# Optimization experiments

Hardware: AMD Instinct MI355X
Metric: run time of the kernel (lower is better)

## Reference

```python
import jax, jax.numpy as jnp
import numpy as np

N_LEVELS = 16
LOG2_T = 19
TABLE_SIZE = 1 << LOG2_T
F_PER_LEVEL = 2
BASE_RES = 16
MAX_RES = 4096
HASH_INIT_SCALE = 0.001
B = 524288

_GROWTH = np.exp((np.log(MAX_RES) - np.log(BASE_RES)) / (N_LEVELS - 1))
SCALINGS = jnp.asarray(np.floor(BASE_RES * _GROWTH ** np.arange(N_LEVELS)), dtype=jnp.float32)  # [L]
HASH_OFFSET = jnp.arange(N_LEVELS, dtype=jnp.int32) * TABLE_SIZE  # [L]
# Instant-NGP spatial hash primes; stored as uint32 so multiplication wraps mod 2^32
# (low 19 bits after xor are identical to torch's int64 computation followed by % 2^19).
PRIMES = jnp.array([1, 2654435761, 805459861], dtype=jnp.uint32)


def _hash_fn(coords_u32):
    # coords_u32: [..., L, 3] uint32 -> [..., L] int32 indices into flat table
    h = coords_u32 * PRIMES
    h = h[..., 0] ^ h[..., 1] ^ h[..., 2]
    h = (h & jnp.uint32(TABLE_SIZE - 1)).astype(jnp.int32)
    return h + HASH_OFFSET


def setup_inputs() -> dict:
    key = jax.random.key(0)
    k1, k2 = jax.random.split(key)
    in_tensor = jax.random.uniform(k1, (B, 3), dtype=jnp.float32)
    hash_table = (jax.random.uniform(k2, (TABLE_SIZE * N_LEVELS, F_PER_LEVEL),
                                     dtype=jnp.float32) * 2.0 - 1.0) * HASH_INIT_SCALE
    return {"in_tensor": in_tensor, "hash_table": hash_table}


def _hashgrid_forward(in_tensor, hash_table):
    # in_tensor: [B, 3] in [0,1]; hash_table: [L*T, F]
    scaled = in_tensor[:, None, :] * SCALINGS[None, :, None]  # [B, L, 3]
    c = jnp.ceil(scaled).astype(jnp.int32)   # ceil corners
    f = jnp.floor(scaled).astype(jnp.int32)  # floor corners
    offset = scaled - f.astype(scaled.dtype)  # [B, L, 3]

    cu = c.astype(jnp.uint32)
    fu = f.astype(jnp.uint32)

    def corner(x, y, z):
        idx = _hash_fn(jnp.stack([x, y, z], axis=-1))  # [B, L]
        return hash_table[idx]  # [B, L, F]

    # Corner ordering exactly as in the torch implementation
    f_0 = corner(cu[..., 0], cu[..., 1], cu[..., 2])
    f_1 = corner(cu[..., 0], fu[..., 1], cu[..., 2])
    f_2 = corner(fu[..., 0], fu[..., 1], cu[..., 2])
    f_3 = corner(fu[..., 0], cu[..., 1], cu[..., 2])
    f_4 = corner(cu[..., 0], cu[..., 1], fu[..., 2])
    f_5 = corner(cu[..., 0], fu[..., 1], fu[..., 2])
    f_6 = corner(fu[..., 0], fu[..., 1], fu[..., 2])
    f_7 = corner(fu[..., 0], cu[..., 1], fu[..., 2])

    ox = offset[..., 0:1]
    oy = offset[..., 1:2]
    oz = offset[..., 2:3]

    f_03 = f_0 * ox + f_3 * (1 - ox)
    f_12 = f_1 * ox + f_2 * (1 - ox)
    f_56 = f_5 * ox + f_6 * (1 - ox)
    f_47 = f_4 * ox + f_7 * (1 - ox)
    f0312 = f_03 * oy + f_12 * (1 - oy)
    f4756 = f_47 * oy + f_56 * (1 - oy)
    enc = f0312 * oz + f4756 * (1 - oz)  # [B, L, F]
    return enc.reshape(enc.shape[0], N_LEVELS * F_PER_LEVEL)  # [B, L*F]


def reference(in_tensor, hash_table):
    # c2f is None -> scale_grad_by_freq is the identity in forward
    return _hashgrid_forward(in_tensor, hash_table)
```

## Files before the change

kernel.cpp:

```cpp
#include <hip/hip_runtime.h>


typedef float f2 __attribute__((ext_vector_type(2)));
typedef float f4 __attribute__((ext_vector_type(4)));

#define TSZ_MASK  ((1u << 19) - 1u)
#define LOG2_B    19

static __constant__ float C_SCALE[16] = {
    16.f,  23.f,  33.f,   48.f,   70.f,   101.f,  147.f,  212.f,
    307.f, 445.f, 645.f,  933.f,  1351.f, 1955.f, 2830.f, 4095.f
};

__global__ __launch_bounds__(256) void hashgrid_gather(
    const float* __restrict__ in,
    const f2*    __restrict__ tab,
    f2*          __restrict__ scratch,
    int lvl0)
{
    const unsigned gid = blockIdx.x * 256 + threadIdx.x;
    const int lvl = lvl0 + (int)(gid >> LOG2_B);
    const unsigned p = gid & TSZ_MASK;

    const float x = __builtin_nontemporal_load(&in[p * 3 + 0]);
    const float y = __builtin_nontemporal_load(&in[p * 3 + 1]);
    const float z = __builtin_nontemporal_load(&in[p * 3 + 2]);
    const float s = C_SCALE[lvl];

    const float sx = x * s, sy = y * s, sz = z * s;
    const float fxf = floorf(sx), fyf = floorf(sy), fzf = floorf(sz);
    const float ox = sx - fxf, oy = sy - fyf, oz = sz - fzf;

    const unsigned fx = (unsigned)(int)fxf;
    const unsigned fy = (unsigned)(int)fyf;
    const unsigned fz = (unsigned)(int)fzf;
    const unsigned cx = (unsigned)(int)ceilf(sx);
    const unsigned cy = (unsigned)(int)ceilf(sy);
    const unsigned cz = (unsigned)(int)ceilf(sz);

    const unsigned hyc = cy * 2654435761u;
    const unsigned hyf = fy * 2654435761u;
    const unsigned hzc = cz * 805459861u;
    const unsigned hzf = fz * 805459861u;

    const f2* __restrict__ tl = tab + ((size_t)lvl << LOG2_B);

    const unsigned i0 = (cx ^ hyc ^ hzc) & TSZ_MASK;
    const unsigned i1 = (cx ^ hyf ^ hzc) & TSZ_MASK;
    const unsigned i2 = (fx ^ hyf ^ hzc) & TSZ_MASK;
    const unsigned i3 = (fx ^ hyc ^ hzc) & TSZ_MASK;
    const unsigned i4 = (cx ^ hyc ^ hzf) & TSZ_MASK;
    const unsigned i5 = (cx ^ hyf ^ hzf) & TSZ_MASK;
    const unsigned i6 = (fx ^ hyf ^ hzf) & TSZ_MASK;
    const unsigned i7 = (fx ^ hyc ^ hzf) & TSZ_MASK;

    const f2 f0 = tl[i0];
    const f2 f1 = tl[i1];
    const f2 f2_ = tl[i2];
    const f2 f3 = tl[i3];
    const f2 f4_ = tl[i4];
    const f2 f5 = tl[i5];
    const f2 f6 = tl[i6];
    const f2 f7 = tl[i7];

    const float rx = 1.f - ox, ry = 1.f - oy, rz = 1.f - oz;
    f2 e = ((f0 * ox + f3 * rx) * oy + (f1 * ox + f2_ * rx) * ry) * oz
         + ((f4_ * ox + f7 * rx) * oy + (f5 * ox + f6 * rx) * ry) * rz;

    __builtin_nontemporal_store(e, &scratch[((size_t)lvl << LOG2_B) + p]);
}

__global__ __launch_bounds__(256) void hashgrid_transpose(
    const f2* __restrict__ scratch,
    f4*       __restrict__ out)
{
    __shared__ f2 tile[64][17];
    const int t = threadIdx.x;
    const int lane = t & 63, w = t >> 6;
    const unsigned pbase = blockIdx.x * 64;

#pragma unroll
    for (int i = 0; i < 4; ++i) {
        const int lvl = w * 4 + i;
        tile[lane][lvl] = __builtin_nontemporal_load(
            &scratch[((size_t)lvl << LOG2_B) + pbase + lane]);
    }
    __syncthreads();

    const unsigned obase = blockIdx.x * 512;
#pragma unroll
    for (int rep = 0; rep < 2; ++rep) {
        const int j = t + rep * 256;
        const int pt = j >> 3, k = j & 7;
        const f2 a = tile[pt][2 * k];
        const f2 b = tile[pt][2 * k + 1];
        f4 v = {a.x, a.y, b.x, b.y};
        __builtin_nontemporal_store(v, &out[obase + j]);
    }
}

__global__ __launch_bounds__(256) void hashgrid_mono(
    const float* __restrict__ in, const f2* __restrict__ tab,
    f2* __restrict__ out, int nthreads)
{
    const int gid = blockIdx.x * 256 + threadIdx.x;
    if (gid >= nthreads) return;
    const int p = gid >> 4;
    const int lvl = gid & 15;

    const float x = in[p * 3 + 0];
    const float y = in[p * 3 + 1];
    const float z = in[p * 3 + 2];
    const float s = C_SCALE[lvl];

    const float sx = x * s, sy = y * s, sz = z * s;
    const float fxf = floorf(sx), fyf = floorf(sy), fzf = floorf(sz);
    const float ox = sx - fxf, oy = sy - fyf, oz = sz - fzf;

    const unsigned fx = (unsigned)(int)fxf, fy = (unsigned)(int)fyf,
                   fz = (unsigned)(int)fzf;
    const unsigned cx = (unsigned)(int)ceilf(sx), cy = (unsigned)(int)ceilf(sy),
                   cz = (unsigned)(int)ceilf(sz);

    const unsigned hyc = cy * 2654435761u, hyf = fy * 2654435761u;
    const unsigned hzc = cz * 805459861u,  hzf = fz * 805459861u;
    const unsigned base = (unsigned)lvl << 19;

    const unsigned i0 = ((cx ^ hyc ^ hzc) & TSZ_MASK) + base;
    const unsigned i1 = ((cx ^ hyf ^ hzc) & TSZ_MASK) + base;
    const unsigned i2 = ((fx ^ hyf ^ hzc) & TSZ_MASK) + base;
    const unsigned i3 = ((fx ^ hyc ^ hzc) & TSZ_MASK) + base;
    const unsigned i4 = ((cx ^ hyc ^ hzf) & TSZ_MASK) + base;
    const unsigned i5 = ((cx ^ hyf ^ hzf) & TSZ_MASK) + base;
    const unsigned i6 = ((fx ^ hyf ^ hzf) & TSZ_MASK) + base;
    const unsigned i7 = ((fx ^ hyc ^ hzf) & TSZ_MASK) + base;

    const f2 f0 = tab[i0], f1 = tab[i1], f2_ = tab[i2], f3 = tab[i3];
    const f2 f4_ = tab[i4], f5 = tab[i5], f6 = tab[i6], f7 = tab[i7];

    const float rx = 1.f - ox, ry = 1.f - oy, rz = 1.f - oz;
    f2 e = ((f0 * ox + f3 * rx) * oy + (f1 * ox + f2_ * rx) * ry) * oz
         + ((f4_ * ox + f7 * rx) * oy + (f5 * ox + f6 * rx) * ry) * rz;

    out[(p << 4) + lvl] = e;
}

extern "C" void kernel_launch(void* const* d_in, const int* in_sizes, int n_in,
                              void* d_out, int out_size, void* d_ws, size_t ws_size,
                              hipStream_t stream)
{
    const float* in  = (const float*)d_in[0];
    const f2*    tab = (const f2*)d_in[1];

    const int n_points = in_sizes[0] / 3;
    const size_t scratch_bytes = (size_t)16 * (1u << LOG2_B) * sizeof(f2);

    if (n_points == (1 << LOG2_B) && ws_size >= scratch_bytes) {
        f2* scratch = (f2*)d_ws;
        hipLaunchKernelGGL(hashgrid_gather, dim3((5u << LOG2_B) / 256), dim3(256),
                           0, stream, in, tab, scratch, 0);
        for (int l = 5; l < 16; ++l) {
            hipLaunchKernelGGL(hashgrid_gather, dim3((1u << LOG2_B) / 256), dim3(256),
                               0, stream, in, tab, scratch, l);
        }
        hipLaunchKernelGGL(hashgrid_transpose, dim3((1u << LOG2_B) / 64), dim3(256),
                           0, stream, scratch, (f4*)d_out);
    } else {
        const int nthreads = n_points * 16;
        hipLaunchKernelGGL(hashgrid_mono, dim3((nthreads + 255) / 256), dim3(256),
                           0, stream, in, tab, (f2*)d_out, nthreads);
    }
}
```

Measured before the change: 298.2 us.

## Merge per-level gather launches into one grid with two points per thread

Replaces the twelve gather launches (levels 0-4 together, then one per level) with a single launch of 16K blocks ordered level-major, where each thread handles two points of the same level. The two corner-index computations run before both trilinear gathers, so sixteen independent table loads are in flight per thread. This removes launch gaps between levels and raises memory-level parallelism. The risk is that all levels now run concurrently, so the L2 working set may grow, and register pressure rises. Corner hashing and interpolation are also factored into shared helpers that the fallback kernel reuses.

```diff
diff --git a/kernel.cpp b/kernel.cpp
--- a/kernel.cpp
+++ b/kernel.cpp
@@ -12,24 +12,20 @@
     307.f, 445.f, 645.f,  933.f,  1351.f, 1955.f, 2830.f, 4095.f
 };
 
-__global__ __launch_bounds__(256) void hashgrid_gather(
-    const float* __restrict__ in,
-    const f2*    __restrict__ tab,
-    f2*          __restrict__ scratch,
-    int lvl0)
+struct Corner8 { unsigned i[8]; float ox, oy, oz; };
+
+__device__ __forceinline__ Corner8 corner_idx(const float* __restrict__ in,
+                                              unsigned p, float s)
 {
-    const unsigned gid = blockIdx.x * 256 + threadIdx.x;
-    const int lvl = lvl0 + (int)(gid >> LOG2_B);
-    const unsigned p = gid & TSZ_MASK;
-
     const float x = __builtin_nontemporal_load(&in[p * 3 + 0]);
     const float y = __builtin_nontemporal_load(&in[p * 3 + 1]);
     const float z = __builtin_nontemporal_load(&in[p * 3 + 2]);
-    const float s = C_SCALE[lvl];
 
     const float sx = x * s, sy = y * s, sz = z * s;
     const float fxf = floorf(sx), fyf = floorf(sy), fzf = floorf(sz);
-    const float ox = sx - fxf, oy = sy - fyf, oz = sz - fzf;
+
+    Corner8 r;
+    r.ox = sx - fxf; r.oy = sy - fyf; r.oz = sz - fzf;
 
     const unsigned fx = (unsigned)(int)fxf;
     const unsigned fy = (unsigned)(int)fyf;
@@ -43,31 +39,46 @@
     const unsigned hzc = cz * 805459861u;
     const unsigned hzf = fz * 805459861u;
 
+    r.i[0] = (cx ^ hyc ^ hzc) & TSZ_MASK;
+    r.i[1] = (cx ^ hyf ^ hzc) & TSZ_MASK;
+    r.i[2] = (fx ^ hyf ^ hzc) & TSZ_MASK;
+    r.i[3] = (fx ^ hyc ^ hzc) & TSZ_MASK;
+    r.i[4] = (cx ^ hyc ^ hzf) & TSZ_MASK;
+    r.i[5] = (cx ^ hyf ^ hzf) & TSZ_MASK;
+    r.i[6] = (fx ^ hyf ^ hzf) & TSZ_MASK;
+    r.i[7] = (fx ^ hyc ^ hzf) & TSZ_MASK;
+    return r;
+}
+
+__device__ __forceinline__ f2 trilerp(const f2* __restrict__ tl, const Corner8& c)
+{
+    const f2 f0 = tl[c.i[0]], f1 = tl[c.i[1]], f2_ = tl[c.i[2]], f3 = tl[c.i[3]];
+    const f2 f4_ = tl[c.i[4]], f5 = tl[c.i[5]], f6 = tl[c.i[6]], f7 = tl[c.i[7]];
+    const float rx = 1.f - c.ox, ry = 1.f - c.oy, rz = 1.f - c.oz;
+    return ((f0 * c.ox + f3 * rx) * c.oy + (f1 * c.ox + f2_ * rx) * ry) * c.oz
+         + ((f4_ * c.ox + f7 * rx) * c.oy + (f5 * c.ox + f6 * rx) * ry) * rz;
+}
+
+__global__ __launch_bounds__(256) void hashgrid_gather(
+    const float* __restrict__ in,
+    const f2*    __restrict__ tab,
+    f2*          __restrict__ scratch)
+{
+    const unsigned b = blockIdx.x;
+    const int lvl = (int)(b >> 10);
+    const unsigned p0 = (b & 1023u) * 512u + threadIdx.x;
+    const unsigned p1 = p0 + 256u;
+    const float s = C_SCALE[lvl];
     const f2* __restrict__ tl = tab + ((size_t)lvl << LOG2_B);
 
-    const unsigned i0 = (cx ^ hyc ^ hzc) & TSZ_MASK;
-    const unsigned i1 = (cx ^ hyf ^ hzc) & TSZ_MASK;
-    const unsigned i2 = (fx ^ hyf ^ hzc) & TSZ_MASK;
-    const unsigned i3 = (fx ^ hyc ^ hzc) & TSZ_MASK;
-    const unsigned i4 = (cx ^ hyc ^ hzf) & TSZ_MASK;
-    const unsigned i5 = (cx ^ hyf ^ hzf) & TSZ_MASK;
-    const unsigned i6 = (fx ^ hyf ^ hzf) & TSZ_MASK;
-    const unsigned i7 = (fx ^ hyc ^ hzf) & TSZ_MASK;
+    const Corner8 ca = corner_idx(in, p0, s);
+    const Corner8 cb = corner_idx(in, p1, s);
+    const f2 ea = trilerp(tl, ca);
+    const f2 eb = trilerp(tl, cb);
 
-    const f2 f0 = tl[i0];
-    const f2 f1 = tl[i1];
-    const f2 f2_ = tl[i2];
-    const f2 f3 = tl[i3];
-    const f2 f4_ = tl[i4];
-    const f2 f5 = tl[i5];
-    const f2 f6 = tl[i6];
-    const f2 f7 = tl[i7];
-
-    const float rx = 1.f - ox, ry = 1.f - oy, rz = 1.f - oz;
-    f2 e = ((f0 * ox + f3 * rx) * oy + (f1 * ox + f2_ * rx) * ry) * oz
-         + ((f4_ * ox + f7 * rx) * oy + (f5 * ox + f6 * rx) * ry) * rz;
-
-    __builtin_nontemporal_store(e, &scratch[((size_t)lvl << LOG2_B) + p]);
+    f2* __restrict__ sl = scratch + ((size_t)lvl << LOG2_B);
+    __builtin_nontemporal_store(ea, &sl[p0]);
+    __builtin_nontemporal_store(eb, &sl[p1]);
 }
 
 __global__ __launch_bounds__(256) void hashgrid_transpose(
@@ -107,42 +118,10 @@
     if (gid >= nthreads) return;
     const int p = gid >> 4;
     const int lvl = gid & 15;
-
-    const float x = in[p * 3 + 0];
-    const float y = in[p * 3 + 1];
-    const float z = in[p * 3 + 2];
     const float s = C_SCALE[lvl];
-
-    const float sx = x * s, sy = y * s, sz = z * s;
-    const float fxf = floorf(sx), fyf = floorf(sy), fzf = floorf(sz);
-    const float ox = sx - fxf, oy = sy - fyf, oz = sz - fzf;
-
-    const unsigned fx = (unsigned)(int)fxf, fy = (unsigned)(int)fyf,
-                   fz = (unsigned)(int)fzf;
-    const unsigned cx = (unsigned)(int)ceilf(sx), cy = (unsigned)(int)ceilf(sy),
-                   cz = (unsigned)(int)ceilf(sz);
-
-    const unsigned hyc = cy * 2654435761u, hyf = fy * 2654435761u;
-    const unsigned hzc = cz * 805459861u,  hzf = fz * 805459861u;
-    const unsigned base = (unsigned)lvl << 19;
-
-    const unsigned i0 = ((cx ^ hyc ^ hzc) & TSZ_MASK) + base;
-    const unsigned i1 = ((cx ^ hyf ^ hzc) & TSZ_MASK) + base;
-    const unsigned i2 = ((fx ^ hyf ^ hzc) & TSZ_MASK) + base;
-    const unsigned i3 = ((fx ^ hyc ^ hzc) & TSZ_MASK) + base;
-    const unsigned i4 = ((cx ^ hyc ^ hzf) & TSZ_MASK) + base;
-    const unsigned i5 = ((cx ^ hyf ^ hzf) & TSZ_MASK) + base;
-    const unsigned i6 = ((fx ^ hyf ^ hzf) & TSZ_MASK) + base;
-    const unsigned i7 = ((fx ^ hyc ^ hzf) & TSZ_MASK) + base;
-
-    const f2 f0 = tab[i0], f1 = tab[i1], f2_ = tab[i2], f3 = tab[i3];
-    const f2 f4_ = tab[i4], f5 = tab[i5], f6 = tab[i6], f7 = tab[i7];
-
-    const float rx = 1.f - ox, ry = 1.f - oy, rz = 1.f - oz;
-    f2 e = ((f0 * ox + f3 * rx) * oy + (f1 * ox + f2_ * rx) * ry) * oz
-         + ((f4_ * ox + f7 * rx) * oy + (f5 * ox + f6 * rx) * ry) * rz;
-
-    out[(p << 4) + lvl] = e;
+    const Corner8 c = corner_idx(in, p, s);
+    const f2* __restrict__ tl = tab + ((size_t)lvl << LOG2_B);
+    out[(p << 4) + lvl] = trilerp(tl, c);
 }
 
 extern "C" void kernel_launch(void* const* d_in, const int* in_sizes, int n_in,
@@ -157,12 +136,8 @@
 
     if (n_points == (1 << LOG2_B) && ws_size >= scratch_bytes) {
         f2* scratch = (f2*)d_ws;
-        hipLaunchKernelGGL(hashgrid_gather, dim3((5u << LOG2_B) / 256), dim3(256),
-                           0, stream, in, tab, scratch, 0);
-        for (int l = 5; l < 16; ++l) {
-            hipLaunchKernelGGL(hashgrid_gather, dim3((1u << LOG2_B) / 256), dim3(256),
-                               0, stream, in, tab, scratch, l);
-        }
+        hipLaunchKernelGGL(hashgrid_gather, dim3(16 * 1024), dim3(256),
+                           0, stream, in, tab, scratch);
         hipLaunchKernelGGL(hashgrid_transpose, dim3((1u << LOG2_B) / 64), dim3(256),
                            0, stream, scratch, (f4*)d_out);
     } else {
```

After: 286.3 us. 1.04x faster.
